# Kernel optimization log

Hardware: AMD Instinct MI355X
Metric: run time of the kernel (lower is better)

The kernel has to match this reference:

```python
import jax, jax.numpy as jnp
import numpy as np

B, L, D, N_HEADS = 8, 512, 1024, 16
D_HEAD = D // N_HEADS


def _mha_fuzzy(x_q, x_k, x_v, Wq, bq, Wk, bk, Wv, bv, Wo, bo):
    """Multi-head fuzzy attention, product t-norm score function."""
    b, lq, d_model = x_q.shape
    lk = x_k.shape[1]

    def proj(x, W, bias, l):
        # [b, l, D] -> [b, h, l, d_head]
        return (x @ W + bias).reshape(b, l, N_HEADS, D_HEAD).transpose(0, 2, 1, 3)

    Q = proj(x_q, Wq, bq, lq)
    K = proj(x_k, Wk, bk, lk)
    V = proj(x_v, Wv, bv, lk)
    # fuzzy memberships in [0,1]
    mu_q = jax.nn.sigmoid(Q)
    mu_k = jax.nn.sigmoid(K)
    # product t-norm aggregated over feature dim (mean), then softmax normalize
    scores = jnp.einsum('bhid,bhjd->bhij', mu_q, mu_k) / D_HEAD  # [b,h,lq,lk]
    attn = jax.nn.softmax(scores, axis=-1)
    out = jnp.einsum('bhij,bhjd->bhid', attn, V)
    out = out.transpose(0, 2, 1, 3).reshape(b, lq, d_model)
    return out @ Wo + bo, attn.mean(axis=1)  # avg over heads


def setup_inputs() -> dict:
    key = jax.random.key(0)
    ks = jax.random.split(key, 16)
    s = 1.0 / np.sqrt(D)
    inp = {
        'text_features': jax.random.normal(ks[0], (B, L, D), jnp.float32),
        'image_features': jax.random.normal(ks[1], (B, L, D), jnp.float32),
        'Wq': jax.random.normal(ks[2], (D, D), jnp.float32) * s,
        'bq': jnp.zeros((D,), jnp.float32),
        'Wk': jax.random.normal(ks[3], (D, D), jnp.float32) * s,
        'bk': jnp.zeros((D,), jnp.float32),
        'Wv': jax.random.normal(ks[4], (D, D), jnp.float32) * s,
        'bv': jnp.zeros((D,), jnp.float32),
        'Wo': jax.random.normal(ks[5], (D, D), jnp.float32) * s,
        'bo': jnp.zeros((D,), jnp.float32),
        'W1': jax.random.normal(ks[6], (3 * D, D), jnp.float32) * (1.0 / np.sqrt(3 * D)),
        'b1': jnp.zeros((D,), jnp.float32),
        'W2': jax.random.normal(ks[7], (D, D), jnp.float32) * s,
        'b2': jnp.zeros((D,), jnp.float32),
    }
    return inp


def reference(text_features, image_features, Wq, bq, Wk, bk, Wv, bv, Wo, bo, W1, b1, W2, b2):
    # shared fuzzy attention module applied in both cross-modal directions
    text_cross, avg_attn = _mha_fuzzy(text_features, image_features, image_features,
                                      Wq, bq, Wk, bk, Wv, bv, Wo, bo)
    image_cross, _ = _mha_fuzzy(image_features, text_features, text_features,
                                Wq, bq, Wk, bk, Wv, bv, Wo, bo)
    combined = jnp.concatenate([text_features, image_features, text_cross], axis=-1)
    hidden = jax.nn.relu(combined @ W1 + b1)
    compositional_output = hidden @ W2 + b2
    return text_cross, image_cross, compositional_output, avg_attn
```

## Files before the change

kernel.cpp:

```cpp
#include <hip/hip_runtime.h>

#define NB 8
#define SL 512
#define DM 1024
#define NH 16
#define DH 64

using bfrag = __attribute__((ext_vector_type(8))) short;
using facc  = __attribute__((ext_vector_type(4))) float;

__device__ __forceinline__ float bf2f(ushort u) {
    return __uint_as_float(((unsigned)u) << 16);
}
__device__ __forceinline__ ushort f2bf(float f) {
    unsigned x = __float_as_uint(f);
    return (ushort)((x + 0x7FFFu + ((x >> 16) & 1u)) >> 16);
}
__device__ __forceinline__ unsigned pack2(float a, float b) {
    return (unsigned)f2bf(a) | ((unsigned)f2bf(b) << 16);
}
__device__ __forceinline__ void gload16(const ushort* g, ushort* l) {
    __builtin_amdgcn_global_load_lds(
        (const __attribute__((address_space(1))) unsigned*)g,
        (__attribute__((address_space(3))) unsigned*)l, 16, 0, 0);
}

__device__ __forceinline__ void tconv_body(const float* __restrict__ W,
                                           ushort* __restrict__ WT,
                                           const int R, const int C,
                                           const int c0, const int r0) {
    __shared__ ushort T[64][68];
    const int tid = threadIdx.x;
    #pragma unroll
    for (int rr = 0; rr < 4; ++rr) {
        const int r = (tid >> 4) + rr * 16;
        const int c4 = (tid & 15) * 4;
        const float4 f = *(const float4*)(W + (size_t)(r0 + r) * C + c0 + c4);
        T[c4+0][r] = f2bf(f.x); T[c4+1][r] = f2bf(f.y);
        T[c4+2][r] = f2bf(f.z); T[c4+3][r] = f2bf(f.w);
    }
    __syncthreads();
    #pragma unroll
    for (int rr = 0; rr < 4; ++rr) {
        const int c = (tid >> 4) + rr * 16;
        const int r4 = (tid & 15) * 4;
        *(ushort4*)(WT + (size_t)(c0 + c) * R + r0 + r4) =
            make_ushort4(T[c][r4+0], T[c][r4+1], T[c][r4+2], T[c][r4+3]);
    }
}

__global__ __launch_bounds__(256)
void prep_k(const float* __restrict__ text, const float* __restrict__ image,
            const float* __restrict__ Wq, const float* __restrict__ Wk,
            const float* __restrict__ Wv, const float* __restrict__ Wo,
            ushort* __restrict__ xbf, ushort* __restrict__ Wt,
            ushort* __restrict__ WoT)
{
    const int bid = blockIdx.x;
    const size_t SZc = (size_t)NB * SL * DM;
    if (bid < 8192) {
        const int half = bid >> 12;
        const float* s = half ? image : text;
        ushort* d = xbf + (size_t)half * SZc;
        const size_t i = ((size_t)(bid & 4095) * 256 + threadIdx.x) * 4;
        const float4 f = *(const float4*)(s + i);
        *(ushort4*)(d + i) =
            make_ushort4(f2bf(f.x), f2bf(f.y), f2bf(f.z), f2bf(f.w));
    } else {
        const int t = bid - 8192;
        const int wsel = t >> 8, tt = t & 255;
        const float* W = (wsel == 0) ? Wq : (wsel == 1) ? Wk
                       : (wsel == 2) ? Wv : Wo;
        ushort* WT = (wsel < 3) ? Wt + (size_t)wsel * DM * DM : WoT;
        tconv_body(W, WT, DM, DM, (tt & 15) * 64, (tt >> 4) * 64);
    }
}

__global__ __launch_bounds__(256)
void tconvW12_k(const float* __restrict__ W1, const float* __restrict__ W2,
                ushort* __restrict__ W1T, ushort* __restrict__ W2T)
{
    const int bid = blockIdx.x;
    if (bid < 768)
        tconv_body(W1, W1T, 3 * DM, DM, (bid & 15) * 64, (bid >> 4) * 64);
    else {
        const int t = bid - 768;
        tconv_body(W2, W2T, DM, DM, (t & 15) * 64, (t >> 4) * 64);
    }
}

template<int ACT, int OMODE>
__global__ __launch_bounds__(256, 2)
void mfma_gemm(const ushort* __restrict__ A0, const ushort* __restrict__ A1,
               const float* __restrict__ A2f, const ushort* __restrict__ A2b,
               const int KA1, const int KA2, const int Ktot,
               const int lda, const int ldaf,
               const ushort* __restrict__ AM1, const int Msplit,
               const ushort* __restrict__ BT, const int ldb,
               const float* __restrict__ bias, const float* __restrict__ biasK,
               const float* __restrict__ biasV,
               float* __restrict__ outf, ushort* __restrict__ outb,
               ushort* __restrict__ outbK, ushort* __restrict__ outbVT,
               const int clustN)
{
    __shared__ ushort sh[32768];
    const int tid  = threadIdx.x;
    const int w    = tid >> 6;
    const int lane = tid & 63;
    const int ln   = lane & 15, qd = lane >> 4;
    const int wm = (w & 1) * 64, wn = (w >> 1) * 64;

    const int NTg = gridDim.x, MTg = gridDim.y;
    const int L   = blockIdx.x + NTg * blockIdx.y;
    const int xcd = L & 7, sIdx = L >> 3;
    int mt, nt;
    if (clustN) { const int np = NTg >> 3; nt = xcd * np + sIdx % np; mt = sIdx / np; }
    else        { mt = xcd * (MTg >> 3) + sIdx / NTg; nt = sIdx - (sIdx / NTg) * NTg; }
    const int m0 = mt * 128, n0 = nt * 128;

    const ushort* A0u = A0; const ushort* A1u = A1; int m0A = m0;
    if (Msplit && m0 >= Msplit) { A0u = AM1; A1u = AM1; m0A = m0 - Msplit; }

    const int arow = (lane >> 3);
    const int kc8s = ((lane & 7) ^ arow) * 8;

    facc acc[4][4];
    #pragma unroll
    for (int i = 0; i < 4; ++i)
        #pragma unroll
        for (int j = 0; j < 4; ++j)
            acc[i][j] = (facc){0.f, 0.f, 0.f, 0.f};

    auto stage = [&](int k0, ushort* buf) {
        ushort* Asb = buf;
        ushort* Bsb = buf + 8192;
        #pragma unroll
        for (int t = 0; t < 4; ++t) {
            const int c = w * 4 + t;
            gload16(BT + (size_t)(n0 + c * 8 + arow) * ldb + k0 + kc8s,
                    &Bsb[c * 512]);
        }
        if (k0 < KA2) {
            const ushort* Ab; int ko;
            if (k0 < KA1) { Ab = A0u; ko = k0; }
            else          { Ab = A1u; ko = k0 - KA1; }
            #pragma unroll
            for (int t = 0; t < 4; ++t) {
                const int c = w * 4 + t;
                gload16(Ab + (size_t)(m0A + c * 8 + arow) * lda + ko + kc8s,
                        &Asb[c * 512]);
            }
        } else if (A2b) {
            const int ko = k0 - KA2;
            #pragma unroll
            for (int t = 0; t < 4; ++t) {
                const int c = w * 4 + t;
                gload16(A2b + (size_t)(m0A + c * 8 + arow) * ldaf + ko + kc8s,
                        &Asb[c * 512]);
            }
        } else {
            const int ko = k0 - KA2;
            #pragma unroll
            for (int t = 0; t < 4; ++t) {
                const int c = w * 4 + t;
                const float* src = A2f + (size_t)(m0A + c * 8 + arow) * ldaf + ko + kc8s;
                const float4 f0 = *(const float4*)src;
                const float4 f1 = *(const float4*)(src + 4);
                uint4 p;
                p.x = pack2(f0.x, f0.y); p.y = pack2(f0.z, f0.w);
                p.z = pack2(f1.x, f1.y); p.w = pack2(f1.z, f1.w);
                *(uint4*)&Asb[c * 512 + lane * 8] = p;
            }
        }
    };

    stage(0, sh);
    for (int k0 = 0; k0 < Ktot; k0 += 64) {
        ushort* cur = sh + ((k0 >> 6) & 1) * 16384;
        ushort* nxt = sh + (((k0 >> 6) & 1) ^ 1) * 16384;
        __syncthreads();
        if (k0 + 64 < Ktot) stage(k0 + 64, nxt);
        ushort* Asb = cur;
        ushort* Bsb = cur + 8192;
        #pragma unroll
        for (int ks = 0; ks < 2; ++ks) {
            const int ch = (ks * 4 + qd) ^ (ln & 7);
            bfrag af[4], bfv[4];
            #pragma unroll
            for (int i = 0; i < 4; ++i)
                af[i] = *(const bfrag*)&Asb[(wm + i*16 + ln) * 64 + ch * 8];
            #pragma unroll
            for (int j = 0; j < 4; ++j)
                bfv[j] = *(const bfrag*)&Bsb[(wn + j*16 + ln) * 64 + ch * 8];
            #pragma unroll
            for (int i = 0; i < 4; ++i)
                #pragma unroll
                for (int j = 0; j < 4; ++j)
                    acc[i][j] = __builtin_amdgcn_mfma_f32_16x16x32_bf16(
                        af[i], bfv[j], acc[i][j], 0, 0, 0);
        }
    }

    if (OMODE == 4) {
        const int seg   = n0 >> 10;
        const int nloc0 = n0 & 1023;
        const float* bs = (seg == 0) ? bias : (seg == 1) ? biasK : biasV;
        if (seg < 2) {
            ushort* ob = (seg == 0) ? outb : outbK;
            #pragma unroll
            for (int j = 0; j < 4; ++j) {
                const int nl = nloc0 + wn + j * 16 + ln;
                const float bn = bs[nl];
                #pragma unroll
                for (int i = 0; i < 4; ++i) {
                    const int mb = m0 + wm + i * 16 + qd * 4;
                    #pragma unroll
                    for (int r = 0; r < 4; ++r) {
                        const float v = 1.f / (1.f + __expf(-(acc[i][j][r] + bn)));
                        const int m = mb + r;
                        const int g = m >> 9, l = m & 511;
                        ob[(((size_t)(g * NH + (nl >> 6))) * SL + l) * DH + (nl & 63)]
                            = f2bf(v);
                    }
                }
            }
        } else {
            __syncthreads();
            #pragma unroll
            for (int j = 0; j < 4; ++j) {
                const int n_l = wn + j * 16 + ln;
                const float bn = bs[nloc0 + n_l];
                #pragma unroll
                for (int i = 0; i < 4; ++i) {
                    #pragma unroll
                    for (int r = 0; r < 4; ++r) {
                        const int m_l = wm + i * 16 + qd * 4 + r;
                        const int c = (m_l >> 3) ^ (n_l & 7);
                        sh[n_l * 128 + c * 8 + (m_l & 7)] = f2bf(acc[i][j][r] + bn);
                    }
                }
            }
            __syncthreads();
            const int n_l = tid >> 1, half = tid & 1;
            const int nl = nloc0 + n_l;
            const int g = m0 >> 9, l0 = m0 & 511;
            ushort* dst = outbVT +
                (((size_t)(g * NH + (nl >> 6))) * DH + (nl & 63)) * SL + l0;
            #pragma unroll
            for (int u = 0; u < 8; ++u) {
                const int c = half * 8 + u;
                const int cs = c ^ (n_l & 7);
                *(uint4*)(dst + c * 8) = *(const uint4*)&sh[n_l * 128 + cs * 8];
            }
        }
        return;
    }

    #pragma unroll
    for (int j = 0; j < 4; ++j) {
        const int n = n0 + wn + j * 16 + ln;
        const float bn = bias[n];
        #pragma unroll
        for (int i = 0; i < 4; ++i) {
            const int mb = m0 + wm + i * 16 + qd * 4;
            #pragma unroll
            for (int r = 0; r < 4; ++r) {
                float v = acc[i][j][r] + bn;
                if (ACT == 1)      v = 1.f / (1.f + __expf(-v));
                else if (ACT == 2) v = v > 0.f ? v : 0.f;
                const int m = mb + r;
                if (OMODE == 0)      outf[(size_t)m * DM + n] = v;
                else if (OMODE == 2) outb[(size_t)m * DM + n] = f2bf(v);
                else {
                    outf[(size_t)m * DM + n] = v;
                    if (m < Msplit) outb[(size_t)m * DM + n] = f2bf(v);
                }
            }
        }
    }
}

__global__ __launch_bounds__(256, 2)
void attn2m_k(const ushort* __restrict__ Qm, const ushort* __restrict__ Km,
              const ushort* __restrict__ VTm, ushort* __restrict__ AO0,
              ushort* __restrict__ AO1, float* __restrict__ RS0,
              float* __restrict__ RS1)
{
    __shared__ ushort Ks[128 * 64];
    __shared__ ushort VTs[64 * 128];
    __shared__ ushort Es[128 * 128];
    const int tid  = threadIdx.x;
    const int w    = tid >> 6;
    const int lane = tid & 63;
    const int ln   = lane & 15, qd = lane >> 4;
    const int wm  = (w & 1) * 64;
    const int wns = (w >> 1) * 64;
    const int wnd = (w >> 1) * 32;

    const int L   = blockIdx.x;
    const int xcd = L & 7, s = L >> 3;
    const int qt  = s & 3;
    const int pid = xcd * 32 + (s >> 2);
    const int h   = pid & 15;
    const int zz  = pid >> 4;
    const int dir = zz >> 3, b = zz & 7;

    const size_t HALFc = (size_t)NB * SL * DM;
    const ushort* Qall = Qm  + (dir ? HALFc : 0);
    const ushort* Kall = Km  + (dir ? 0 : HALFc);
    const ushort* Vall = VTm + (dir ? 0 : HALFc);
    ushort* AOp = dir ? AO1 : AO0;
    float*  RSp = dir ? RS1 : RS0;

    const size_t ho = ((size_t)(b * NH + h)) * SL * DH;
    const ushort* Qg  = Qall + ho + (size_t)qt * 128 * DH;
    const ushort* Kg  = Kall + ho;
    const ushort* VTg = Vall + ho;

    bfrag qf[4][2];
    #pragma unroll
    for (int i = 0; i < 4; ++i)
        #pragma unroll
        for (int ks = 0; ks < 2; ++ks)
            qf[i][ks] = *(const bfrag*)(Qg + (size_t)(wm + i*16 + ln) * DH + ks*32 + qd*8);

    facc oacc[4][2];
    #pragma unroll
    for (int i = 0; i < 4; ++i)
        #pragma unroll
        for (int j = 0; j < 2; ++j)
            oacc[i][j] = (facc){0.f, 0.f, 0.f, 0.f};
    float rp[4];
    #pragma unroll
    for (int i = 0; i < 4; ++i)
        rp[i] = 0.f;

    const int arow = lane >> 3;
    const int kc8s = ((lane & 7) ^ arow) * 8;
    const int vrow = lane >> 4;

    for (int kc = 0; kc < 4; ++kc) {
        __syncthreads();
        #pragma unroll
        for (int t = 0; t < 4; ++t) {
            const int c = w * 4 + t;
            const int vc8s = ((lane & 15) ^ ((c * 4 + vrow) & 7)) * 8;
            gload16(Kg + (size_t)(kc*128 + c*8 + arow) * DH + kc8s, &Ks[c * 512]);
            gload16(VTg + (size_t)(c*4 + vrow) * SL + kc*128 + vc8s, &VTs[c * 512]);
        }
        __syncthreads();

        facc sacc[4][4];
        #pragma unroll
        for (int j = 0; j < 4; ++j)
            #pragma unroll
            for (int i = 0; i < 4; ++i)
                sacc[j][i] = (facc){0.f, 0.f, 0.f, 0.f};
        #pragma unroll
        for (int ks = 0; ks < 2; ++ks) {
            const int ch = (ks * 4 + qd) ^ (ln & 7);
            bfrag kf[4];
            #pragma unroll
            for (int j = 0; j < 4; ++j)
                kf[j] = *(const bfrag*)&Ks[(wns + j*16 + ln) * 64 + ch * 8];
            #pragma unroll
            for (int j = 0; j < 4; ++j)
                #pragma unroll
                for (int i = 0; i < 4; ++i)
                    sacc[j][i] = __builtin_amdgcn_mfma_f32_16x16x32_bf16(
                        kf[j], qf[i][ks], sacc[j][i], 0, 0, 0);
        }

        #pragma unroll
        for (int i = 0; i < 4; ++i) {
            const int q  = wm + i*16 + ln;
            const int qs = q & 7;
            float p = 0.f;
            #pragma unroll
            for (int j = 0; j < 4; ++j) {
                const int key0 = wns + j*16 + qd*4;
                const float e0 = __expf(sacc[j][i][0] * 0.015625f);
                const float e1 = __expf(sacc[j][i][1] * 0.015625f);
                const float e2 = __expf(sacc[j][i][2] * 0.015625f);
                const float e3 = __expf(sacc[j][i][3] * 0.015625f);
                const int c = ((key0 & 127) >> 3) ^ qs;
                uint2 pk;
                pk.x = pack2(e0, e1);
                pk.y = pack2(e2, e3);
                *(uint2*)&Es[q * 128 + c * 8 + (key0 & 7)] = pk;
                p += (e0 + e1) + (e2 + e3);
            }
            rp[i] += p;
        }
        __syncthreads();

        #pragma unroll
        for (int ks2 = 0; ks2 < 4; ++ks2) {
            const int vch = (ks2 * 4 + qd) ^ (ln & 7);
            bfrag ea[4], vb[2];
            #pragma unroll
            for (int i = 0; i < 4; ++i) {
                const int q = wm + i*16 + ln;
                const int cs = (ks2*4 + qd) ^ (q & 7);
                ea[i] = *(const bfrag*)&Es[q * 128 + cs * 8];
            }
            #pragma unroll
            for (int j = 0; j < 2; ++j)
                vb[j] = *(const bfrag*)&VTs[(wnd + j*16 + ln) * 128 + vch * 8];
            #pragma unroll
            for (int i = 0; i < 4; ++i)
                #pragma unroll
                for (int j = 0; j < 2; ++j)
                    oacc[i][j] = __builtin_amdgcn_mfma_f32_16x16x32_bf16(
                        ea[i], vb[j], oacc[i][j], 0, 0, 0);
        }
    }

    #pragma unroll
    for (int i = 0; i < 4; ++i) {
        float p = rp[i];
        p += __shfl_xor(p, 16);
        p += __shfl_xor(p, 32);
        rp[i] = p;
    }

    __syncthreads();
    float* rsls = (float*)Ks;
    if (qd == 0) {
        #pragma unroll
        for (int i = 0; i < 4; ++i)
            rsls[(w >> 1) * 128 + wm + i*16 + ln] = rp[i];
    }
    __syncthreads();
    if (tid < 128) {
        const float t = rsls[tid] + rsls[128 + tid];
        RSp[(size_t)(b * NH + h) * SL + qt * 128 + tid] = t;
        rsls[tid] = t;
    }
    __syncthreads();

    #pragma unroll
    for (int i = 0; i < 4; ++i) {
        #pragma unroll
        for (int r = 0; r < 4; ++r) {
            const int q = wm + i*16 + qd*4 + r;
            const float inv = 1.f / rsls[q];
            const size_t rowo = ((size_t)(b*SL + qt*128 + q)) * DM + h*DH;
            #pragma unroll
            for (int j = 0; j < 2; ++j)
                AOp[rowo + wnd + j*16 + ln] = f2bf(oacc[i][j][r] * inv);
        }
    }
}

__global__ __launch_bounds__(256, 2)
void avg3_k(const ushort* __restrict__ Qm, const ushort* __restrict__ Km,
            const float* __restrict__ RS, float* __restrict__ avga)
{
    __shared__ ushort Qs[64 * 64];
    __shared__ ushort Kt[64 * 64];
    __shared__ float rss[64];
    const int tid  = threadIdx.x;
    const int w    = tid >> 6;
    const int lane = tid & 63;
    const int ln   = lane & 15, qd = lane >> 4;
    const int wq = (w & 1) * 32, wk = (w >> 1) * 32;
    const int kt = blockIdx.x, qt = blockIdx.y, b = blockIdx.z;

    const int arow = lane >> 3;
    const int kc8s = ((lane & 7) ^ arow) * 8;

    float acc[2][2][4];
    #pragma unroll
    for (int i = 0; i < 2; ++i)
        #pragma unroll
        for (int j = 0; j < 2; ++j)
            #pragma unroll
            for (int r = 0; r < 4; ++r)
                acc[i][j][r] = 0.f;

    for (int h = 0; h < NH; ++h) {
        const size_t ho = ((size_t)(b * NH + h)) * SL * DH;
        __syncthreads();
        #pragma unroll
        for (int t = 0; t < 2; ++t) {
            const int c = w * 2 + t;
            gload16(Qm + ho + (size_t)(qt*64 + c*8 + arow) * DH + kc8s, &Qs[c * 512]);
            gload16(Km + ho + (size_t)(kt*64 + c*8 + arow) * DH + kc8s, &Kt[c * 512]);
        }
        if (tid < 64) rss[tid] = RS[(size_t)(b*NH + h)*SL + qt*64 + tid];
        __syncthreads();

        facc s[2][2];
        #pragma unroll
        for (int i = 0; i < 2; ++i)
            #pragma unroll
            for (int j = 0; j < 2; ++j)
                s[i][j] = (facc){0.f, 0.f, 0.f, 0.f};
        #pragma unroll
        for (int ks = 0; ks < 2; ++ks) {
            const int ch = (ks * 4 + qd) ^ (ln & 7);
            bfrag qa[2], kb[2];
            #pragma unroll
            for (int i = 0; i < 2; ++i)
                qa[i] = *(const bfrag*)&Qs[(wq + i*16 + ln) * 64 + ch * 8];
            #pragma unroll
            for (int j = 0; j < 2; ++j)
                kb[j] = *(const bfrag*)&Kt[(wk + j*16 + ln) * 64 + ch * 8];
            #pragma unroll
            for (int i = 0; i < 2; ++i)
                #pragma unroll
                for (int j = 0; j < 2; ++j)
                    s[i][j] = __builtin_amdgcn_mfma_f32_16x16x32_bf16(
                        qa[i], kb[j], s[i][j], 0, 0, 0);
        }
        #pragma unroll
        for (int i = 0; i < 2; ++i) {
            #pragma unroll
            for (int r = 0; r < 4; ++r) {
                const float ir = 0.0625f / rss[wq + i*16 + qd*4 + r];
                #pragma unroll
                for (int j = 0; j < 2; ++j)
                    acc[i][j][r] += __expf(s[i][j][r] * 0.015625f) * ir;
            }
        }
    }
    #pragma unroll
    for (int i = 0; i < 2; ++i) {
        #pragma unroll
        for (int r = 0; r < 4; ++r) {
            const int q = wq + i*16 + qd*4 + r;
            #pragma unroll
            for (int j = 0; j < 2; ++j)
                avga[((size_t)(b*SL + qt*64 + q)) * SL + kt*64 + wk + j*16 + ln]
                    = acc[i][j][r];
        }
    }
}

extern "C" void kernel_launch(void* const* d_in, const int* in_sizes, int n_in,
                              void* d_out, int out_size, void* d_ws, size_t ws_size,
                              hipStream_t stream)
{
    (void)in_sizes; (void)n_in; (void)out_size;
    const float* text  = (const float*)d_in[0];
    const float* image = (const float*)d_in[1];
    const float* Wq = (const float*)d_in[2];
    const float* bq = (const float*)d_in[3];
    const float* Wk = (const float*)d_in[4];
    const float* bk = (const float*)d_in[5];
    const float* Wv = (const float*)d_in[6];
    const float* bv = (const float*)d_in[7];
    const float* Wo = (const float*)d_in[8];
    const float* bo = (const float*)d_in[9];
    const float* W1 = (const float*)d_in[10];
    const float* b1 = (const float*)d_in[11];
    const float* W2 = (const float*)d_in[12];
    const float* b2 = (const float*)d_in[13];
    float* out = (float*)d_out;

    const size_t SZ   = (size_t)NB * SL * DM;
    const size_t HALF = SZ;

    ushort* xbf = (ushort*)d_ws;
    ushort* Qb  = xbf + 2*SZ;
    ushort* Kb  = Qb  + 2*SZ;
    ushort* VT  = Kb  + 2*SZ;
    ushort* AOt = VT  + 2*SZ;
    ushort* Wt  = AOt + SZ;
    float*  RS  = (float*)(Wt + 3*DM*DM);
    char*   wsEnd = (char*)(RS + NB*NH*SL);
    ushort* hidden = Qb;
    ushort* W2T    = AOt;

    float* text_cross = out;
    float* comp       = out + 2*SZ;
    float* avga       = out + 3*SZ;

    const size_t extBytes = (size_t)NB*NH*SL*4 + (size_t)DM*DM*2 + (size_t)SZ*2;
    const size_t fixBytes = (size_t)(wsEnd - (char*)d_ws);
    float* RS2; ushort* WoT; ushort* AOi;
    if (ws_size >= fixBytes + extBytes) {
        RS2 = (float*)wsEnd;
        WoT = (ushort*)(RS2 + NB*NH*SL);
        AOi = WoT + DM*DM;
    } else {
        WoT = (ushort*)comp;
        AOi = WoT + DM*DM;
        RS2 = (float*)Wt;
    }

    const dim3 blk(256);

    prep_k<<<9216, blk, 0, stream>>>(text, image, Wq, Wk, Wv, Wo, xbf, Wt, WoT);

    mfma_gemm<0,4><<<dim3(24,64), blk, 0, stream>>>(
        xbf, xbf, nullptr, nullptr, DM, DM, DM, DM, DM, nullptr, 0,
        Wt, DM, bq, bk, bv, nullptr, Qb, Kb, VT, 1);

    attn2m_k<<<dim3(1024), blk, 0, stream>>>(Qb, Kb, VT, AOt, AOi, RS, RS2);
    avg3_k<<<dim3(SL/64, SL/64, NB), blk, 0, stream>>>(Qb, Kb + HALF, RS, avga);

    mfma_gemm<0,5><<<dim3(8,64), blk, 0, stream>>>(
        AOt, AOt, nullptr, nullptr, DM, DM, DM, DM, DM, AOi, 4096,
        WoT, DM, bo, nullptr, nullptr, text_cross, Kb, nullptr, nullptr, 0);

    tconvW12_k<<<1024, blk, 0, stream>>>(W1, W2, Wt, W2T);

    mfma_gemm<2,2><<<dim3(8,32), blk, 0, stream>>>(
        xbf, xbf + SZ, nullptr, Kb, DM, 2*DM, 3*DM, DM, DM, nullptr, 0,
        Wt, 3*DM, b1, nullptr, nullptr, nullptr, hidden, nullptr, nullptr, 0);
    mfma_gemm<0,0><<<dim3(8,32), blk, 0, stream>>>(
        hidden, hidden, nullptr, nullptr, DM, DM, DM, DM, DM, nullptr, 0,
        W2T, DM, b2, nullptr, nullptr, comp, nullptr, nullptr, nullptr, 0);
}
```

Measured before the change: 338.5 us.

## Fuse out-projection GEMM, head-averaged attention and W1/W2 transpose into one launch

Turns the GEMM, avg-attention and transpose kernels into device-function bodies that take a shared-memory pointer. A new combined kernel dispatches on block index: even and odd blocks interleave the output-projection GEMM with the head-averaged attention, and the remaining blocks do the W1/W2 transpose-convert. W2T moves to its own workspace slot when workspace allows, so the transpose does not overwrite AOt while the GEMM still reads it. The aim is to cut two launches and the tail idle time between independent stages. The cost is that every block now reserves 64KB of shared memory, including the light transpose and averaging blocks, which may limit how many blocks fit on a CU.

```diff
diff --git a/kernel.cpp b/kernel.cpp
--- a/kernel.cpp
+++ b/kernel.cpp
@@ -25,11 +25,12 @@
         (__attribute__((address_space(3))) unsigned*)l, 16, 0, 0);
 }
 
-__device__ __forceinline__ void tconv_body(const float* __restrict__ W,
+__device__ __forceinline__ void tconv_body(void* smem_,
+                                           const float* __restrict__ W,
                                            ushort* __restrict__ WT,
                                            const int R, const int C,
                                            const int c0, const int r0) {
-    __shared__ ushort T[64][68];
+    ushort (*T)[68] = (ushort (*)[68])smem_;
     const int tid = threadIdx.x;
     #pragma unroll
     for (int rr = 0; rr < 4; ++rr) {
@@ -56,6 +57,7 @@
             ushort* __restrict__ xbf, ushort* __restrict__ Wt,
             ushort* __restrict__ WoT)
 {
+    __shared__ ushort Tbuf[64][68];
     const int bid = blockIdx.x;
     const size_t SZc = (size_t)NB * SL * DM;
     if (bid < 8192) {
@@ -72,7 +74,7 @@
         const float* W = (wsel == 0) ? Wq : (wsel == 1) ? Wk
                        : (wsel == 2) ? Wv : Wo;
         ushort* WT = (wsel < 3) ? Wt + (size_t)wsel * DM * DM : WoT;
-        tconv_body(W, WT, DM, DM, (tt & 15) * 64, (tt >> 4) * 64);
+        tconv_body(Tbuf, W, WT, DM, DM, (tt & 15) * 64, (tt >> 4) * 64);
     }
 }
 
@@ -80,38 +82,38 @@
 void tconvW12_k(const float* __restrict__ W1, const float* __restrict__ W2,
                 ushort* __restrict__ W1T, ushort* __restrict__ W2T)
 {
+    __shared__ ushort Tbuf[64][68];
     const int bid = blockIdx.x;
     if (bid < 768)
-        tconv_body(W1, W1T, 3 * DM, DM, (bid & 15) * 64, (bid >> 4) * 64);
+        tconv_body(Tbuf, W1, W1T, 3 * DM, DM, (bid & 15) * 64, (bid >> 4) * 64);
     else {
         const int t = bid - 768;
-        tconv_body(W2, W2T, DM, DM, (t & 15) * 64, (t >> 4) * 64);
+        tconv_body(Tbuf, W2, W2T, DM, DM, (t & 15) * 64, (t >> 4) * 64);
     }
 }
 
 template<int ACT, int OMODE>
-__global__ __launch_bounds__(256, 2)
-void mfma_gemm(const ushort* __restrict__ A0, const ushort* __restrict__ A1,
-               const float* __restrict__ A2f, const ushort* __restrict__ A2b,
-               const int KA1, const int KA2, const int Ktot,
-               const int lda, const int ldaf,
-               const ushort* __restrict__ AM1, const int Msplit,
-               const ushort* __restrict__ BT, const int ldb,
-               const float* __restrict__ bias, const float* __restrict__ biasK,
-               const float* __restrict__ biasV,
-               float* __restrict__ outf, ushort* __restrict__ outb,
-               ushort* __restrict__ outbK, ushort* __restrict__ outbVT,
-               const int clustN)
-{
-    __shared__ ushort sh[32768];
+__device__ __forceinline__ void gemm_body(
+    void* smem_, const int L, const int NTg, const int MTg,
+    const ushort* __restrict__ A0, const ushort* __restrict__ A1,
+    const float* __restrict__ A2f, const ushort* __restrict__ A2b,
+    const int KA1, const int KA2, const int Ktot,
+    const int lda, const int ldaf,
+    const ushort* __restrict__ AM1, const int Msplit,
+    const ushort* __restrict__ BT, const int ldb,
+    const float* __restrict__ bias, const float* __restrict__ biasK,
+    const float* __restrict__ biasV,
+    float* __restrict__ outf, ushort* __restrict__ outb,
+    ushort* __restrict__ outbK, ushort* __restrict__ outbVT,
+    const int clustN)
+{
+    ushort* sh = (ushort*)smem_;
     const int tid  = threadIdx.x;
     const int w    = tid >> 6;
     const int lane = tid & 63;
     const int ln   = lane & 15, qd = lane >> 4;
     const int wm = (w & 1) * 64, wn = (w >> 1) * 64;
 
-    const int NTg = gridDim.x, MTg = gridDim.y;
-    const int L   = blockIdx.x + NTg * blockIdx.y;
     const int xcd = L & 7, sIdx = L >> 3;
     int mt, nt;
     if (clustN) { const int np = NTg >> 3; nt = xcd * np + sIdx % np; mt = sIdx / np; }
@@ -280,6 +282,28 @@
     }
 }
 
+template<int ACT, int OMODE>
+__global__ __launch_bounds__(256, 2)
+void mfma_gemm(const ushort* __restrict__ A0, const ushort* __restrict__ A1,
+               const float* __restrict__ A2f, const ushort* __restrict__ A2b,
+               const int KA1, const int KA2, const int Ktot,
+               const int lda, const int ldaf,
+               const ushort* __restrict__ AM1, const int Msplit,
+               const ushort* __restrict__ BT, const int ldb,
+               const float* __restrict__ bias, const float* __restrict__ biasK,
+               const float* __restrict__ biasV,
+               float* __restrict__ outf, ushort* __restrict__ outb,
+               ushort* __restrict__ outbK, ushort* __restrict__ outbVT,
+               const int clustN)
+{
+    __shared__ char smem[65536];
+    gemm_body<ACT, OMODE>(smem, blockIdx.x + gridDim.x * blockIdx.y,
+                          gridDim.x, gridDim.y,
+                          A0, A1, A2f, A2b, KA1, KA2, Ktot, lda, ldaf,
+                          AM1, Msplit, BT, ldb, bias, biasK, biasV,
+                          outf, outb, outbK, outbVT, clustN);
+}
+
 __global__ __launch_bounds__(256, 2)
 void attn2m_k(const ushort* __restrict__ Qm, const ushort* __restrict__ Km,
               const ushort* __restrict__ VTm, ushort* __restrict__ AO0,
@@ -453,19 +477,21 @@
     }
 }
 
-__global__ __launch_bounds__(256, 2)
-void avg3_k(const ushort* __restrict__ Qm, const ushort* __restrict__ Km,
-            const float* __restrict__ RS, float* __restrict__ avga)
-{
-    __shared__ ushort Qs[64 * 64];
-    __shared__ ushort Kt[64 * 64];
-    __shared__ float rss[64];
+__device__ __forceinline__ void avg3_body(void* smem_, const int kt,
+                                          const int qt, const int b,
+                                          const ushort* __restrict__ Qm,
+                                          const ushort* __restrict__ Km,
+                                          const float* __restrict__ RS,
+                                          float* __restrict__ avga)
+{
+    ushort* Qs = (ushort*)smem_;
+    ushort* Kt = Qs + 64 * 64;
+    float* rss = (float*)(Kt + 64 * 64);
     const int tid  = threadIdx.x;
     const int w    = tid >> 6;
     const int lane = tid & 63;
     const int ln   = lane & 15, qd = lane >> 4;
     const int wq = (w & 1) * 32, wk = (w >> 1) * 32;
-    const int kt = blockIdx.x, qt = blockIdx.y, b = blockIdx.z;
 
     const int arow = lane >> 3;
     const int kc8s = ((lane & 7) ^ arow) * 8;
@@ -534,6 +560,38 @@
             for (int j = 0; j < 2; ++j)
                 avga[((size_t)(b*SL + qt*64 + q)) * SL + kt*64 + wk + j*16 + ln]
                     = acc[i][j][r];
+        }
+    }
+}
+
+__global__ __launch_bounds__(256, 2)
+void mid_k(const ushort* __restrict__ AOt, const ushort* __restrict__ AOi,
+           const ushort* __restrict__ WoT, const float* __restrict__ bo,
+           float* __restrict__ text_cross, ushort* __restrict__ tcb,
+           const ushort* __restrict__ Qm, const ushort* __restrict__ Km,
+           const float* __restrict__ RS, float* __restrict__ avga,
+           const float* __restrict__ W1, const float* __restrict__ W2,
+           ushort* __restrict__ W1T, ushort* __restrict__ W2T)
+{
+    __shared__ char smem[65536];
+    const int bid = blockIdx.x;
+    if (bid < 1024) {
+        if (bid & 1) {
+            const int la = bid >> 1;
+            avg3_body(smem, la & 7, (la >> 3) & 7, la >> 6, Qm, Km, RS, avga);
+        } else {
+            gemm_body<0, 5>(smem, bid >> 1, 8, 64,
+                AOt, AOt, nullptr, nullptr, DM, DM, DM, DM, DM,
+                AOi, 4096, WoT, DM, bo, nullptr, nullptr,
+                text_cross, tcb, nullptr, nullptr, 0);
+        }
+    } else {
+        const int t = bid - 1024;
+        if (t < 768)
+            tconv_body(smem, W1, W1T, 3 * DM, DM, (t & 15) * 64, (t >> 4) * 64);
+        else {
+            const int u = t - 768;
+            tconv_body(smem, W2, W2T, DM, DM, (u & 15) * 64, (u >> 4) * 64);
         }
     }
 }
@@ -571,23 +629,26 @@
     float*  RS  = (float*)(Wt + 3*DM*DM);
     char*   wsEnd = (char*)(RS + NB*NH*SL);
     ushort* hidden = Qb;
-    ushort* W2T    = AOt;
 
     float* text_cross = out;
     float* comp       = out + 2*SZ;
     float* avga       = out + 3*SZ;
 
-    const size_t extBytes = (size_t)NB*NH*SL*4 + (size_t)DM*DM*2 + (size_t)SZ*2;
+    const size_t extBytes = (size_t)NB*NH*SL*4 + (size_t)DM*DM*2
+                          + (size_t)SZ*2 + (size_t)DM*DM*2;
     const size_t fixBytes = (size_t)(wsEnd - (char*)d_ws);
-    float* RS2; ushort* WoT; ushort* AOi;
-    if (ws_size >= fixBytes + extBytes) {
+    float* RS2; ushort* WoT; ushort* AOi; ushort* W2T;
+    const bool ext = (ws_size >= fixBytes + extBytes);
+    if (ext) {
         RS2 = (float*)wsEnd;
         WoT = (ushort*)(RS2 + NB*NH*SL);
         AOi = WoT + DM*DM;
+        W2T = AOi + SZ;
     } else {
         WoT = (ushort*)comp;
         AOi = WoT + DM*DM;
         RS2 = (float*)Wt;
+        W2T = AOt;
     }
 
     const dim3 blk(256);
@@ -599,13 +660,15 @@
         Wt, DM, bq, bk, bv, nullptr, Qb, Kb, VT, 1);
 
     attn2m_k<<<dim3(1024), blk, 0, stream>>>(Qb, Kb, VT, AOt, AOi, RS, RS2);
-    avg3_k<<<dim3(SL/64, SL/64, NB), blk, 0, stream>>>(Qb, Kb + HALF, RS, avga);
-
-    mfma_gemm<0,5><<<dim3(8,64), blk, 0, stream>>>(
-        AOt, AOt, nullptr, nullptr, DM, DM, DM, DM, DM, AOi, 4096,
-        WoT, DM, bo, nullptr, nullptr, text_cross, Kb, nullptr, nullptr, 0);
-
-    tconvW12_k<<<1024, blk, 0, stream>>>(W1, W2, Wt, W2T);
+
+    if (ext) {
+        mid_k<<<2048, blk, 0, stream>>>(AOt, AOi, WoT, bo, text_cross, Kb,
+                                        Qb, Kb + HALF, RS, avga, W1, W2, Wt, W2T);
+    } else {
+        mid_k<<<1024, blk, 0, stream>>>(AOt, AOi, WoT, bo, text_cross, Kb,
+                                        Qb, Kb + HALF, RS, avga, W1, W2, Wt, W2T);
+        tconvW12_k<<<1024, blk, 0, stream>>>(W1, W2, Wt, W2T);
+    }
 
     mfma_gemm<2,2><<<dim3(8,32), blk, 0, stream>>>(
         xbf, xbf + SZ, nullptr, Kb, DM, 2*DM, 3*DM, DM, DM, nullptr, 0,
```

New measurement: 332.2 us. About the same (-1.8%).
